# Optimization experiments

Hardware: AMD Instinct MI355X
Metric: run time of the kernel (lower is better)

Reference implementation:

```python
import jax, jax.numpy as jnp
import numpy as np

N = 100000
E = 1600000
D = 128          # in_feat == hidden_size
L = 3            # hidden layers
EPS = 1e-5       # BatchNorm1d eps


def setup_inputs() -> dict:
    key = jax.random.key(0)
    ks = jax.random.split(key, 12)
    x = jax.random.normal(ks[0], (N, D), dtype=jnp.float32)
    edge_index = jax.random.randint(ks[1], (2, E), 0, N, dtype=jnp.int64)
    s = 1.0 / np.sqrt(D)
    # stacked hidden-layer SAGEConv params: lin_l (neighbor), lin_r (root), bias on lin_l
    Wl = jax.random.uniform(ks[2], (L, D, D), jnp.float32, -s, s)
    Wr = jax.random.uniform(ks[3], (L, D, D), jnp.float32, -s, s)
    b = jax.random.uniform(ks[4], (L, D), jnp.float32, -s, s)
    # batchnorm affine params
    gamma = jnp.ones((L, D), jnp.float32)
    beta = jnp.zeros((L, D), jnp.float32)
    # output SAGEConv: D -> 1
    Wl_out = jax.random.uniform(ks[5], (D, 1), jnp.float32, -s, s)
    Wr_out = jax.random.uniform(ks[6], (D, 1), jnp.float32, -s, s)
    b_out = jax.random.uniform(ks[7], (1,), jnp.float32, -s, s)
    return {"x": x, "edge_index": edge_index, "Wl": Wl, "Wr": Wr, "b": b,
            "gamma": gamma, "beta": beta, "Wl_out": Wl_out, "Wr_out": Wr_out,
            "b_out": b_out}


def _sage(x, src, dst, inv_deg, Wl, Wr, b):
    # gather neighbor features along edges, mean-aggregate at destination
    msg_sum = jax.ops.segment_sum(x[src], dst, num_segments=N)   # [N, F]
    mean = msg_sum * inv_deg                                     # 0 for isolated nodes
    return mean @ Wl + x @ Wr + b


def _batchnorm(x, gamma, beta):
    m = jnp.mean(x, axis=0)
    v = jnp.mean((x - m) ** 2, axis=0)  # biased var, as torch BN uses for normalization
    return gamma * (x - m) * jax.lax.rsqrt(v + EPS) + beta


def reference(x, edge_index, Wl, Wr, b, gamma, beta, Wl_out, Wr_out, b_out):
    src, dst = edge_index[0], edge_index[1]
    deg = jax.ops.segment_sum(jnp.ones((E,), x.dtype), dst, num_segments=N)
    inv_deg = jnp.where(deg > 0, 1.0 / jnp.maximum(deg, 1.0), 0.0)[:, None]
    h = x
    for i in range(L):
        h = _sage(h, src, dst, inv_deg, Wl[i], Wr[i], b[i])
        h = jax.nn.relu(h)
        h = _batchnorm(h, gamma[i], beta[i])
    out = _sage(h, src, dst, inv_deg, Wl_out, Wr_out, b_out)
    return jax.nn.sigmoid(out)  # [N, 1]
```

## Files before the change

### kernel.cpp

```cpp
#include <hip/hip_runtime.h>

typedef unsigned short u16;
typedef unsigned int u32;
typedef unsigned long long u64;

#define GN 100000
#define GE 1600000
#define DCAP 64
#define NRANGE 196
#define NBKT (NRANGE * 8)
#define BCAP 1536
#define LDA 136

typedef __bf16 bf16x8 __attribute__((ext_vector_type(8)));
typedef float f32x4 __attribute__((ext_vector_type(4)));
typedef float f32x2 __attribute__((ext_vector_type(2)));
typedef u32 u32x4 __attribute__((ext_vector_type(4)));
typedef u32 u32x2 __attribute__((ext_vector_type(2)));

__device__ __forceinline__ float bl(u32 u){ return __uint_as_float(u << 16); }
__device__ __forceinline__ float bh(u32 u){ return __uint_as_float(u & 0xffff0000u); }
__device__ __forceinline__ float bfu(u16 v){ return __uint_as_float(((u32)v) << 16); }
__device__ __forceinline__ u16 f2bf(float f){
    u32 u = __float_as_uint(f);
    u32 r = (u + 0x7fffu + ((u >> 16) & 1u)) >> 16;
    return (u16)r;
}
__device__ __forceinline__ u32 pack2(float a, float b){
    return (u32)f2bf(a) | ((u32)f2bf(b) << 16);
}
__device__ __forceinline__ u32 pk8x4(float a, float b, float c, float d){
    u32 p = (u32)__builtin_amdgcn_cvt_pk_fp8_f32(a, b, 0, false);
    p = (u32)__builtin_amdgcn_cvt_pk_fp8_f32(c, d, p, true);
    return p;
}

__global__ void __launch_bounds__(256) k_init(const int* ei, const u32* xraw,
                                              int* cursor, float* colpart, int* flags,
                                              int* bcur){
    int i = blockIdx.x * 256 + threadIdx.x;
    if (i < GN) cursor[i] = 0;
    if (i < NBKT) bcur[i] = 0;
    if (i < 6144) colpart[i] = 0.f;
    int t = threadIdx.x;
    if (blockIdx.x == 0){
        __shared__ int s_any[4];
        int v = 0;
        #pragma unroll
        for (int j = 0; j < 4; ++j){
            int k = t * 4 + j;
            v |= ei[2 * k * 1000 + 1];
        }
        #pragma unroll
        for (int m = 1; m < 64; m <<= 1) v |= __shfl_xor(v, m);
        if ((t & 63) == 0) s_any[t >> 6] = v;
        __syncthreads();
        if (t == 0){
            int any = s_any[0] | s_any[1] | s_any[2] | s_any[3];
            flags[0] = (any == 0) ? 1 : 0;
        }
    }
    if (blockIdx.x == 1){
        __shared__ int s_cnt[4];
        int cnt = 0;
        #pragma unroll
        for (int j = 0; j < 4; ++j){
            int idx = (t * 4 + j) * 6000 + 3;
            u32 u = xraw[idx];
            int e = (u >> 7) & 0xFF;
            cnt += (e >= 100 && e <= 140) ? 1 : 0;
        }
        #pragma unroll
        for (int m = 1; m < 64; m <<= 1) cnt += __shfl_xor(cnt, m);
        if ((t & 63) == 0) s_cnt[t >> 6] = cnt;
        __syncthreads();
        if (t == 0){
            int tot = s_cnt[0] + s_cnt[1] + s_cnt[2] + s_cnt[3];
            flags[1] = (tot > 512) ? 0 : 1;
        }
    }
}

__global__ void __launch_bounds__(256) k_convx(const void* x, const int* flags,
                                               u16* xb, u32* h8){
    int tid = blockIdx.x * 256 + threadIdx.x;
    int node = tid >> 4, l15 = tid & 15;
    if (node >= GN) return;
    float f[8];
    if (flags[1]){
        const float* xf = (const float*)x + node * 128 + l15;
        #pragma unroll
        for (int a = 0; a < 8; ++a) f[a] = __builtin_nontemporal_load(xf + a * 16);
    } else {
        const u16* xh = (const u16*)x + node * 128 + l15;
        #pragma unroll
        for (int a = 0; a < 8; ++a) f[a] = bfu(xh[a * 16]);
    }
    u16* xo = xb + node * 128 + l15;
    #pragma unroll
    for (int a = 0; a < 8; ++a) xo[a * 16] = f2bf(f[a]);
    u32x2 e = { pk8x4(f[0], f[1], f[2], f[3]), pk8x4(f[4], f[5], f[6], f[7]) };
    ((u32x2*)h8)[node * 16 + l15] = e;
}

#define WOFF_WR    49152
#define WOFF_B     98304
#define WOFF_G     98688
#define WOFF_BE    99072
#define WOFF_WLO   99456
#define WOFF_WRO   99584
#define WOFF_BO    99712
#define WTOT       99713
__global__ void __launch_bounds__(256) k_convw(const void* Wl, const void* Wr, const void* b,
                                               const void* g, const void* be, const void* wlo,
                                               const void* wro, const void* bo,
                                               const int* flags, u16* wbuf, float* biasf){
    int i = blockIdx.x * 256 + threadIdx.x;
    if (i >= WTOT) return;
    const void* s; int k;
    if (i < WOFF_B){
        bool isWl = (i < WOFF_WR);
        const void* src = isWl ? Wl : Wr;
        int r = isWl ? i : i - WOFF_WR;
        int layer = r >> 14, L = r & 16383;
        int kk = isWl ? (((L & 7) << 4) | (L >> 10))
                      : (((L >> 10) << 3) | (L & 7));
        int cc = (L >> 3) & 127;
        int si = layer * 16384 + kk * 128 + cc;
        float fv = flags[1] ? ((const float*)src)[si] : bfu(((const u16*)src)[si]);
        wbuf[i] = f2bf(fv);
        return;
    }
    if      (i < WOFF_G  ){ s = b;   k = i - WOFF_B; }
    else if (i < WOFF_BE ){ s = g;   k = i - WOFF_G; }
    else if (i < WOFF_WLO){ s = be;  k = i - WOFF_BE; }
    else if (i < WOFF_WRO){ s = wlo; k = i - WOFF_WLO; }
    else if (i < WOFF_BO ){ s = wro; k = i - WOFF_WRO; }
    else                  { s = bo;  k = 0; }
    float fv = flags[1] ? ((const float*)s)[k] : bfu(((const u16*)s)[k]);
    wbuf[i] = f2bf(fv);
    if (i >= WOFF_B && i < WOFF_B + 384) biasf[i - WOFF_B] = fv;
}

__global__ void __launch_bounds__(256) k_fillA(const int* ei, const int* flags,
                                               int* bcur, u64* pairs){
    __shared__ int cnt[256];
    __shared__ int lofs[256];
    __shared__ int gbase[NRANGE];
    __shared__ int wsum[4];
    __shared__ u64 lp[1024];
    int t = threadIdx.x;
    int lane = t & 63, w = t >> 6;
    int res = blockIdx.x & 7;
    int base = blockIdx.x * 1024;
    int is64 = flags[0];
    cnt[t] = 0;
    __syncthreads();
    int myd[4], mys[4], slot[4], myr[4];
    #pragma unroll
    for (int j = 0; j < 4; ++j){
        int e = base + j * 256 + t;
        if (e < GE){
            int d, s;
            if (is64){ d = __builtin_nontemporal_load(ei + 2 * (GE + e));
                       s = __builtin_nontemporal_load(ei + 2 * e); }
            else     { d = __builtin_nontemporal_load(ei + GE + e);
                       s = __builtin_nontemporal_load(ei + e); }
            myd[j] = d; mys[j] = s; myr[j] = d >> 9;
            slot[j] = atomicAdd(&cnt[myr[j]], 1);
        } else myr[j] = -1;
    }
    __syncthreads();
    int v = cnt[t];
    int sv = v;
    #pragma unroll
    for (int d = 1; d < 64; d <<= 1){
        int u = __shfl_up(sv, d);
        if (lane >= d) sv += u;
    }
    if (lane == 63) wsum[w] = sv;
    __syncthreads();
    int prefix = 0;
    #pragma unroll
    for (int j = 0; j < 4; ++j) if (j < w) prefix += wsum[j];
    lofs[t] = sv + prefix - v;
    if (t < NRANGE && cnt[t] > 0)
        gbase[t] = atomicAdd(&bcur[t * 8 + res], cnt[t]);
    __syncthreads();
    #pragma unroll
    for (int j = 0; j < 4; ++j){
        if (myr[j] >= 0)
            lp[lofs[myr[j]] + slot[j]] = ((u64)(u32)myd[j] << 32) | (u32)mys[j];
    }
    __syncthreads();
    int total = GE - base; if (total > 1024) total = 1024;
    for (int i = t; i < total; i += 256){
        u64 pr = lp[i];
        int r = (int)(pr >> 32) >> 9;
        int g = gbase[r] + (i - lofs[r]);
        if (g < BCAP) pairs[((size_t)(r * 8 + res)) * BCAP + g] = pr;
    }
}

__global__ void __launch_bounds__(256) k_fillB(const int* bcur, const u64* pairs,
                                               int* cursor, int* col){
    int range = blockIdx.x % 200;
    int sub   = blockIdx.x / 200;
    if (range >= NRANGE || sub >= 8) return;
    int bkt = range * 8 + sub;
    int n = bcur[bkt]; if (n > BCAP) n = BCAP;
    const u64* P = pairs + (size_t)bkt * BCAP;
    for (int i = threadIdx.x; i < n; i += 256){
        u64 pr = __builtin_nontemporal_load(P + i);
        int s = (int)(u32)pr, d = (int)(pr >> 32);
        int pos = atomicAdd(&cursor[d], 1);
        if (pos < DCAP) col[d * DCAP + pos] = s;
    }
}

__global__ void __launch_bounds__(256, 4) k_gemm(const u32* h8, const int* deg, const int* col,
                                                 const u16* hin,
                                                 const u16* Wlp, const u16* Wrp,
                                                 const float* biasf, u16* hout,
                                                 u32* h8o, int write8, float* colpart){
    __shared__ u16 smA[128 * LDA];
    __shared__ float sst[256];
    int t = threadIdx.x;
    int wid = t >> 6, lane = t & 63;
    int quad = lane >> 4, l15 = lane & 15;
    int r0 = blockIdx.x * 128;
    sst[t] = 0.f;

    {
        int g = t >> 4, lg = t & 15;
        const u32x2* hrow = (const u32x2*)h8;
        #define ACC8(v) { \
            A01 += __builtin_amdgcn_cvt_pk_f32_fp8((v).x, false); \
            A23 += __builtin_amdgcn_cvt_pk_f32_fp8((v).x, true);  \
            A45 += __builtin_amdgcn_cvt_pk_f32_fp8((v).y, false); \
            A67 += __builtin_amdgcn_cvt_pk_f32_fp8((v).y, true); }
        for (int m = 0; m < 8; ++m){
            int lr = g + (m << 4);
            int node = r0 + lr;
            f32x2 A01 = {0.f,0.f}, A23 = {0.f,0.f}, A45 = {0.f,0.f}, A67 = {0.f,0.f};
            int d = 0;
            if (node < GN){
                d = deg[node];
                int cnt = d < DCAP ? d : DCAP;
                const int* nb = col + node * DCAP;
                int e = 0;
                for (; e + 7 < cnt; e += 8){
                    u32x2 v0 = hrow[(size_t)nb[e]     * 16 + lg];
                    u32x2 v1 = hrow[(size_t)nb[e + 1] * 16 + lg];
                    u32x2 v2 = hrow[(size_t)nb[e + 2] * 16 + lg];
                    u32x2 v3 = hrow[(size_t)nb[e + 3] * 16 + lg];
                    u32x2 v4 = hrow[(size_t)nb[e + 4] * 16 + lg];
                    u32x2 v5 = hrow[(size_t)nb[e + 5] * 16 + lg];
                    u32x2 v6 = hrow[(size_t)nb[e + 6] * 16 + lg];
                    u32x2 v7 = hrow[(size_t)nb[e + 7] * 16 + lg];
                    ACC8(v0) ACC8(v1) ACC8(v2) ACC8(v3) ACC8(v4) ACC8(v5) ACC8(v6) ACC8(v7)
                }
                for (; e + 1 < cnt; e += 2){
                    u32x2 v0 = hrow[(size_t)nb[e]     * 16 + lg];
                    u32x2 v1 = hrow[(size_t)nb[e + 1] * 16 + lg];
                    ACC8(v0) ACC8(v1)
                }
                if (e < cnt){
                    u32x2 v0 = hrow[(size_t)nb[e] * 16 + lg];
                    ACC8(v0)
                }
            }
            float inv = (d > 0) ? 1.f / (float)d : 0.f;
            f32x2 iv = {inv, inv};
            A01 *= iv; A23 *= iv; A45 *= iv; A67 *= iv;
            u32x4 o;
            o.x = pack2(A01.x, A01.y); o.y = pack2(A23.x, A23.y);
            o.z = pack2(A45.x, A45.y); o.w = pack2(A67.x, A67.y);
            *(u32x4*)(smA + lr * LDA + lg * 8) = o;
        }
        #undef ACC8
    }
    __syncthreads();

    f32x4 acc[2][8];
    #pragma unroll
    for (int i = 0; i < 2; i++)
        #pragma unroll
        for (int j = 0; j < 8; j++) acc[i][j] = (f32x4){0.f, 0.f, 0.f, 0.f};

    int node0 = r0 + wid * 32 + l15, node1 = node0 + 16;

    {
        const u32x4* Wg = (const u32x4*)Wlp;
        const u16* a0 = smA + (wid * 32 + l15) * LDA;
        const u16* a1 = a0 + 16 * LDA;
        #pragma unroll
        for (int s = 0; s < 4; ++s){
            int kc = (s << 2) + quad;
            union { u32x4 u; bf16x8 v; } fa0, fa1;
            fa0.u = *(const u32x4*)(a0 + (kc << 3));
            fa1.u = *(const u32x4*)(a1 + (kc << 3));
            const u32x4* wg = Wg + (kc << 7) + l15;
            #pragma unroll
            for (int cb = 0; cb < 8; ++cb){
                union { u32x4 u; bf16x8 v; } fw;
                fw.u = wg[cb << 4];
                acc[0][cb] = __builtin_amdgcn_mfma_f32_16x16x32_bf16(fa0.v, fw.v, acc[0][cb], 0, 0, 0);
                acc[1][cb] = __builtin_amdgcn_mfma_f32_16x16x32_bf16(fa1.v, fw.v, acc[1][cb], 0, 0, 0);
            }
        }
    }
    {
        const u32x4* Wg = (const u32x4*)Wrp;
        #pragma unroll
        for (int s = 0; s < 4; ++s){
            int kk = (s << 5) + (quad << 3);
            union { u32x4 u; bf16x8 v; } fa0, fa1;
            fa0.u = (node0 < GN) ? *(const u32x4*)(hin + node0 * 128 + kk) : (u32x4){0,0,0,0};
            fa1.u = (node1 < GN) ? *(const u32x4*)(hin + node1 * 128 + kk) : (u32x4){0,0,0,0};
            int kc = (s << 2) + quad;
            const u32x4* wg = Wg + (kc << 7) + l15;
            #pragma unroll
            for (int cb = 0; cb < 8; ++cb){
                union { u32x4 u; bf16x8 v; } fw;
                fw.u = wg[cb << 4];
                acc[0][cb] = __builtin_amdgcn_mfma_f32_16x16x32_bf16(fa0.v, fw.v, acc[0][cb], 0, 0, 0);
                acc[1][cb] = __builtin_amdgcn_mfma_f32_16x16x32_bf16(fa1.v, fw.v, acc[1][cb], 0, 0, 0);
            }
        }
    }

    float bsv[8];
    #pragma unroll
    for (int cb = 0; cb < 8; cb++) bsv[cb] = biasf[cb * 16 + l15];
    float csum[8], csq[8];
    #pragma unroll
    for (int cb = 0; cb < 8; cb++){ csum[cb] = 0.f; csq[cb] = 0.f; }

    #pragma unroll
    for (int rb = 0; rb < 2; ++rb){
        #pragma unroll
        for (int rr = 0; rr < 4; ++rr){
            int row = r0 + wid * 32 + rb * 16 + quad * 4 + rr;
            float v[8];
            #pragma unroll
            for (int cb = 0; cb < 8; ++cb) v[cb] = fmaxf(acc[rb][cb][rr] + bsv[cb], 0.f);
            if (row < GN){
                #pragma unroll
                for (int cb = 0; cb < 8; ++cb){
                    hout[row * 128 + cb * 16 + l15] = f2bf(v[cb]);
                    csum[cb] += v[cb]; csq[cb] += v[cb] * v[cb];
                }
                if (write8){
                    u32x2 pp = { pk8x4(v[0], v[1], v[2], v[3]),
                                 pk8x4(v[4], v[5], v[6], v[7]) };
                    ((u32x2*)h8o)[row * 16 + l15] = pp;
                }
            }
        }
    }
    #pragma unroll
    for (int cb = 0; cb < 8; cb++){
        float cs = csum[cb], cq = csq[cb];
        cs += __shfl_xor(cs, 16); cs += __shfl_xor(cs, 32);
        cq += __shfl_xor(cq, 16); cq += __shfl_xor(cq, 32);
        if (quad == 0){
            atomicAdd(&sst[cb * 16 + l15], cs);
            atomicAdd(&sst[128 + cb * 16 + l15], cq);
        }
    }
    __syncthreads();
    atomicAdd(&colpart[(blockIdx.x & 7) * 256 + t], sst[t]);
}

__global__ void __launch_bounds__(256) k_bnf(const float* colpart, const u16* gamma, const u16* beta,
                                             int mode,
                                             const u16* WlN, const u16* WrN, u16* wfd,
                                             const float* bNsrc, float* bNdst,
                                             const u16* wlo, const u16* wro, const u16* bo,
                                             u16* hwl, u16* hwr, float* hb){
    __shared__ float s_sc[128], s_sh[128], s_red[256];
    int t = threadIdx.x, b = blockIdx.x;
    if (t < 128){
        float s = 0.f, q = 0.f;
        #pragma unroll
        for (int j = 0; j < 8; ++j){
            s += colpart[j * 256 + t];
            q += colpart[j * 256 + 128 + t];
        }
        const float invn = 1.f / (float)GN;
        float mean = s * invn;
        float var = fmaxf(q * invn - mean * mean, 0.f);
        float rstd = rsqrtf(var + 1e-5f);
        float g  = bfu(gamma[t]);
        float be = bfu(beta[t]);
        float sc = g * rstd, sh = be - mean * sc;
        s_sc[t] = sc; s_sh[t] = sh;
    }
    __syncthreads();
    if (mode == 0){
        if (b < 64){
            int idx = b * 256 + t;
            int kl = ((idx & 7) << 4) | (idx >> 10);
            int kr = ((idx >> 10) << 3) | (idx & 7);
            wfd[idx]         = f2bf(s_sc[kl] * bfu(WlN[idx]));
            wfd[16384 + idx] = f2bf(s_sc[kr] * bfu(WrN[idx]));
        } else if (t < 128){
            float acc = bNsrc[t];
            for (int k = 0; k < 128; ++k){
                int Ll = ((k & 15) << 10) + (t << 3) + (k >> 4);
                int Lr = ((k >> 3) << 10) + (t << 3) + (k & 7);
                acc += s_sh[k] * (bfu(WlN[Ll]) + bfu(WrN[Lr]));
            }
            bNdst[t] = acc;
        }
    } else if (b == 64){
        float contrib = 0.f;
        if (t < 128){
            float wl = bfu(wlo[t]), wr = bfu(wro[t]);
            hwl[t] = f2bf(s_sc[t] * wl);
            hwr[t] = f2bf(s_sc[t] * wr);
            contrib = s_sh[t] * (wl + wr);
        }
        s_red[t] = contrib;
        __syncthreads();
        for (int off = 128; off >= 1; off >>= 1){
            if (t < off) s_red[t] += s_red[t + off];
            __syncthreads();
        }
        if (t == 0) hb[0] = s_red[0] + bfu(bo[0]);
    }
}

__global__ void __launch_bounds__(256) k_dot(const u16* h, const u16* wl, const u16* wr,
                                             float* y, float* r){
    int node = (blockIdx.x * 256 + threadIdx.x) >> 6;
    int lane = threadIdx.x & 63;
    if (node >= GN) return;
    u32 hv  = ((const u32*)h)[node * 64 + lane];
    u32 wlv = ((const u32*)wl)[lane];
    u32 wrv = ((const u32*)wr)[lane];
    float hlo = bl(hv), hhi = bh(hv);
    float ya = hlo * bl(wlv) + hhi * bh(wlv);
    float ra = hlo * bl(wrv) + hhi * bh(wrv);
    #pragma unroll
    for (int m = 1; m < 64; m <<= 1){ ya += __shfl_xor(ya, m); ra += __shfl_xor(ra, m); }
    if (lane == 0){ y[node] = ya; r[node] = ra; }
}

__global__ void __launch_bounds__(256) k_out(const float* y, const float* r, const int* deg,
                                             const int* col, const float* hb,
                                             const int* flags, void* out){
    int n = blockIdx.x * 256 + threadIdx.x;
    if (n >= GN) return;
    int d = deg[n];
    int cnt = d < DCAP ? d : DCAP;
    const int* nb = col + n * DCAP;
    float s = 0.f;
    for (int e = 0; e < cnt; ++e) s += y[nb[e]];
    float inv = (d > 0) ? 1.f / (float)d : 0.f;
    float z = inv * s + r[n] + hb[0];
    float sg = 1.f / (1.f + __expf(-z));
    if (flags[1]) ((float*)out)[n] = sg;
    else          ((u16*)out)[n] = f2bf(sg);
}

extern "C" void kernel_launch(void* const* d_in, const int* in_sizes, int n_in,
                              void* d_out, int out_size, void* d_ws, size_t ws_size,
                              hipStream_t stream) {
    const void* x     = d_in[0];
    const int*  ei    = (const int*)d_in[1];
    const void* Wl    = d_in[2];
    const void* Wr    = d_in[3];
    const void* bias  = d_in[4];
    const void* gamma = d_in[5];
    const void* beta  = d_in[6];
    const void* wlout = d_in[7];
    const void* wrout = d_in[8];
    const void* bout  = d_in[9];

    char* p = (char*)d_ws;
    auto take = [&](size_t b){ void* q = (void*)p; p += (b + 255) & ~(size_t)255; return q; };
    int*   cursor = (int*)  take((size_t)GN * 4);
    int*   flags  = (int*)  take(256);
    int*   bcur   = (int*)  take((size_t)NBKT * 4);
    float* colpart= (float*)take(6144 * 4);
    float* biasf  = (float*)take(384 * 4);
    float* bf2    = (float*)take(128 * 4);
    float* bf3    = (float*)take(128 * 4);
    float* hb     = (float*)take(256);
    u16*   wf2    = (u16*)  take(32768 * 2);
    u16*   wf3    = (u16*)  take(32768 * 2);
    u16*   hwl    = (u16*)  take(128 * 2);
    u16*   hwr    = (u16*)  take(128 * 2);
    float* yv     = (float*)take((size_t)GN * 4);
    float* rv     = (float*)take((size_t)GN * 4);
    int*   col    = (int*)  take((size_t)GN * DCAP * 4);
    u16*   xb     = (u16*)  take((size_t)GN * 128 * 2);
    u16*   hbuf   = (u16*)  take((size_t)GN * 128 * 2);
    u32*   h8a    = (u32*)  take((size_t)GN * 128);
    u32*   h8b    = (u32*)  take((size_t)GN * 128);
    u64*   pairs  = (u64*)  take((size_t)NBKT * BCAP * 8);
    u16*   wbuf   = (u16*)  take((size_t)WTOT * 2);

    const int NB_N = (GN + 255) / 256;
    const int NB_W = (GN + 3) / 4;
    const int NB_G = (GN + 127) / 128;
    const int NB_M = (GN * 16 + 255) / 256;
    const int NB_C = (WTOT + 255) / 256;
    const int NB_A = (GE + 1023) / 1024;

    k_init <<<NB_N, 256, 0, stream>>>(ei, (const u32*)x, cursor, colpart, flags, bcur);
    k_convx<<<NB_M, 256, 0, stream>>>(x, flags, xb, h8a);
    k_convw<<<NB_C, 256, 0, stream>>>(Wl, Wr, bias, gamma, beta, wlout, wrout, bout, flags, wbuf, biasf);
    k_fillA<<<NB_A, 256, 0, stream>>>(ei, flags, bcur, pairs);
    k_fillB<<<1600, 256, 0, stream>>>(bcur, pairs, cursor, col);

    const u16* hin = xb;
    for (int i = 0; i < 3; ++i){
        const u16* Wlp; const u16* Wrp; const float* bfi;
        if (i == 0){ Wlp = wbuf;     Wrp = wbuf + WOFF_WR; bfi = biasf; }
        else if (i == 1){ Wlp = wf2; Wrp = wf2 + 16384;    bfi = bf2; }
        else { Wlp = wf3;            Wrp = wf3 + 16384;    bfi = bf3; }
        u16* wfd = (i == 0) ? wf2 : wf3;
        float* bNdst = (i == 0) ? bf2 : bf3;
        int nx = (i < 2) ? (i + 1) : 0;
        const u32* h8i = (i == 1) ? h8b : h8a;
        u32*       h8o = (i == 0) ? h8b : h8a;
        k_gemm<<<NB_G, 256, 0, stream>>>(h8i, cursor, col, hin, Wlp, Wrp, bfi,
                                         hbuf, (i == 2) ? h8b : h8o, (i < 2) ? 1 : 0,
                                         colpart + i * 2048);
        k_bnf <<<65, 256, 0, stream>>>(colpart + i * 2048,
            wbuf + WOFF_G + i * 128, wbuf + WOFF_BE + i * 128, (i == 2) ? 1 : 0,
            wbuf + nx * 16384, wbuf + WOFF_WR + nx * 16384, wfd,
            biasf + nx * 128, bNdst,
            wbuf + WOFF_WLO, wbuf + WOFF_WRO, wbuf + WOFF_BO, hwl, hwr, hb);
        hin = hbuf;
    }
    k_dot<<<NB_W, 256, 0, stream>>>(hbuf, hwl, hwr, yv, rv);
    k_out<<<NB_N, 256, 0, stream>>>(yv, rv, cursor, col, hb, flags, d_out);
}
```

Measured before the change: 459.0 us.

## Shrink GEMM tile to 64 rows with per-wave gather and no block barriers

Rows per block in the fused aggregate+GEMM kernel drop from 128 to 64. Each wave now gathers its own 16 rows with 16-byte fp8 loads (8 lanes per row), so the LDS tile is wave-private and the __syncthreads becomes a waitcnt. Column statistics are atomically added straight to global partials instead of going through a shared-memory reduction. This lowers LDS use and synchronisation to raise occupancy and latency hiding for the gather. In exchange, each B-fragment load now feeds half as many MFMAs, and there are more global atomics.

```diff
diff --git a/kernel.cpp b/kernel.cpp
--- a/kernel.cpp
+++ b/kernel.cpp
@@ -223,26 +223,31 @@
                                                  const u16* Wlp, const u16* Wrp,
                                                  const float* biasf, u16* hout,
                                                  u32* h8o, int write8, float* colpart){
-    __shared__ u16 smA[128 * LDA];
-    __shared__ float sst[256];
+    __shared__ u16 smA[64 * LDA];
     int t = threadIdx.x;
     int wid = t >> 6, lane = t & 63;
     int quad = lane >> 4, l15 = lane & 15;
-    int r0 = blockIdx.x * 128;
-    sst[t] = 0.f;
+    int r0 = blockIdx.x * 64;
+    int wr0 = wid * 16;
 
     {
-        int g = t >> 4, lg = t & 15;
-        const u32x2* hrow = (const u32x2*)h8;
-        #define ACC8(v) { \
-            A01 += __builtin_amdgcn_cvt_pk_f32_fp8((v).x, false); \
-            A23 += __builtin_amdgcn_cvt_pk_f32_fp8((v).x, true);  \
-            A45 += __builtin_amdgcn_cvt_pk_f32_fp8((v).y, false); \
-            A67 += __builtin_amdgcn_cvt_pk_f32_fp8((v).y, true); }
-        for (int m = 0; m < 8; ++m){
-            int lr = g + (m << 4);
+        int g8 = lane >> 3, lg8 = lane & 7;
+        const u32x4* hrow4 = (const u32x4*)h8;
+        #define ACC16(v) { \
+            a01 += __builtin_amdgcn_cvt_pk_f32_fp8((v).x, false); \
+            a23 += __builtin_amdgcn_cvt_pk_f32_fp8((v).x, true);  \
+            a45 += __builtin_amdgcn_cvt_pk_f32_fp8((v).y, false); \
+            a67 += __builtin_amdgcn_cvt_pk_f32_fp8((v).y, true);  \
+            b01 += __builtin_amdgcn_cvt_pk_f32_fp8((v).z, false); \
+            b23 += __builtin_amdgcn_cvt_pk_f32_fp8((v).z, true);  \
+            b45 += __builtin_amdgcn_cvt_pk_f32_fp8((v).w, false); \
+            b67 += __builtin_amdgcn_cvt_pk_f32_fp8((v).w, true); }
+        #pragma unroll
+        for (int m = 0; m < 2; ++m){
+            int lr = wr0 + (g8 << 1) + m;
             int node = r0 + lr;
-            f32x2 A01 = {0.f,0.f}, A23 = {0.f,0.f}, A45 = {0.f,0.f}, A67 = {0.f,0.f};
+            f32x2 a01 = {0.f,0.f}, a23 = {0.f,0.f}, a45 = {0.f,0.f}, a67 = {0.f,0.f};
+            f32x2 b01 = {0.f,0.f}, b23 = {0.f,0.f}, b45 = {0.f,0.f}, b67 = {0.f,0.f};
             int d = 0;
             if (node < GN){
                 d = deg[node];
@@ -250,63 +255,65 @@
                 const int* nb = col + node * DCAP;
                 int e = 0;
                 for (; e + 7 < cnt; e += 8){
-                    u32x2 v0 = hrow[(size_t)nb[e]     * 16 + lg];
-                    u32x2 v1 = hrow[(size_t)nb[e + 1] * 16 + lg];
-                    u32x2 v2 = hrow[(size_t)nb[e + 2] * 16 + lg];
-                    u32x2 v3 = hrow[(size_t)nb[e + 3] * 16 + lg];
-                    u32x2 v4 = hrow[(size_t)nb[e + 4] * 16 + lg];
-                    u32x2 v5 = hrow[(size_t)nb[e + 5] * 16 + lg];
-                    u32x2 v6 = hrow[(size_t)nb[e + 6] * 16 + lg];
-                    u32x2 v7 = hrow[(size_t)nb[e + 7] * 16 + lg];
-                    ACC8(v0) ACC8(v1) ACC8(v2) ACC8(v3) ACC8(v4) ACC8(v5) ACC8(v6) ACC8(v7)
+                    u32x4 v0 = hrow4[(size_t)nb[e]     * 8 + lg8];
+                    u32x4 v1 = hrow4[(size_t)nb[e + 1] * 8 + lg8];
+                    u32x4 v2 = hrow4[(size_t)nb[e + 2] * 8 + lg8];
+                    u32x4 v3 = hrow4[(size_t)nb[e + 3] * 8 + lg8];
+                    u32x4 v4 = hrow4[(size_t)nb[e + 4] * 8 + lg8];
+                    u32x4 v5 = hrow4[(size_t)nb[e + 5] * 8 + lg8];
+                    u32x4 v6 = hrow4[(size_t)nb[e + 6] * 8 + lg8];
+                    u32x4 v7 = hrow4[(size_t)nb[e + 7] * 8 + lg8];
+                    ACC16(v0) ACC16(v1) ACC16(v2) ACC16(v3)
+                    ACC16(v4) ACC16(v5) ACC16(v6) ACC16(v7)
                 }
                 for (; e + 1 < cnt; e += 2){
-                    u32x2 v0 = hrow[(size_t)nb[e]     * 16 + lg];
-                    u32x2 v1 = hrow[(size_t)nb[e + 1] * 16 + lg];
-                    ACC8(v0) ACC8(v1)
+                    u32x4 v0 = hrow4[(size_t)nb[e]     * 8 + lg8];
+                    u32x4 v1 = hrow4[(size_t)nb[e + 1] * 8 + lg8];
+                    ACC16(v0) ACC16(v1)
                 }
                 if (e < cnt){
-                    u32x2 v0 = hrow[(size_t)nb[e] * 16 + lg];
-                    ACC8(v0)
+                    u32x4 v0 = hrow4[(size_t)nb[e] * 8 + lg8];
+                    ACC16(v0)
                 }
             }
             float inv = (d > 0) ? 1.f / (float)d : 0.f;
             f32x2 iv = {inv, inv};
-            A01 *= iv; A23 *= iv; A45 *= iv; A67 *= iv;
-            u32x4 o;
-            o.x = pack2(A01.x, A01.y); o.y = pack2(A23.x, A23.y);
-            o.z = pack2(A45.x, A45.y); o.w = pack2(A67.x, A67.y);
-            *(u32x4*)(smA + lr * LDA + lg * 8) = o;
-        }
-        #undef ACC8
-    }
-    __syncthreads();
-
-    f32x4 acc[2][8];
-    #pragma unroll
-    for (int i = 0; i < 2; i++)
-        #pragma unroll
-        for (int j = 0; j < 8; j++) acc[i][j] = (f32x4){0.f, 0.f, 0.f, 0.f};
-
-    int node0 = r0 + wid * 32 + l15, node1 = node0 + 16;
+            a01 *= iv; a23 *= iv; a45 *= iv; a67 *= iv;
+            b01 *= iv; b23 *= iv; b45 *= iv; b67 *= iv;
+            u32x4 o0, o1;
+            o0.x = pack2(a01.x, a01.y); o0.y = pack2(a23.x, a23.y);
+            o0.z = pack2(a45.x, a45.y); o0.w = pack2(a67.x, a67.y);
+            o1.x = pack2(b01.x, b01.y); o1.y = pack2(b23.x, b23.y);
+            o1.z = pack2(b45.x, b45.y); o1.w = pack2(b67.x, b67.y);
+            u16* wp = smA + lr * LDA + (lg8 << 4);
+            *(u32x4*)wp = o0;
+            *(u32x4*)(wp + 8) = o1;
+        }
+        #undef ACC16
+    }
+    __asm__ volatile("s_waitcnt lgkmcnt(0)" ::: "memory");
+    __builtin_amdgcn_sched_barrier(0);
+
+    f32x4 acc[8];
+    #pragma unroll
+    for (int j = 0; j < 8; j++) acc[j] = (f32x4){0.f, 0.f, 0.f, 0.f};
+
+    int node0 = r0 + wr0 + l15;
 
     {
         const u32x4* Wg = (const u32x4*)Wlp;
-        const u16* a0 = smA + (wid * 32 + l15) * LDA;
-        const u16* a1 = a0 + 16 * LDA;
+        const u16* a0 = smA + (wr0 + l15) * LDA;
         #pragma unroll
         for (int s = 0; s < 4; ++s){
             int kc = (s << 2) + quad;
-            union { u32x4 u; bf16x8 v; } fa0, fa1;
+            union { u32x4 u; bf16x8 v; } fa0;
             fa0.u = *(const u32x4*)(a0 + (kc << 3));
-            fa1.u = *(const u32x4*)(a1 + (kc << 3));
             const u32x4* wg = Wg + (kc << 7) + l15;
             #pragma unroll
             for (int cb = 0; cb < 8; ++cb){
                 union { u32x4 u; bf16x8 v; } fw;
                 fw.u = wg[cb << 4];
-                acc[0][cb] = __builtin_amdgcn_mfma_f32_16x16x32_bf16(fa0.v, fw.v, acc[0][cb], 0, 0, 0);
-                acc[1][cb] = __builtin_amdgcn_mfma_f32_16x16x32_bf16(fa1.v, fw.v, acc[1][cb], 0, 0, 0);
+                acc[cb] = __builtin_amdgcn_mfma_f32_16x16x32_bf16(fa0.v, fw.v, acc[cb], 0, 0, 0);
             }
         }
     }
@@ -315,17 +322,15 @@
         #pragma unroll
         for (int s = 0; s < 4; ++s){
             int kk = (s << 5) + (quad << 3);
-            union { u32x4 u; bf16x8 v; } fa0, fa1;
+            union { u32x4 u; bf16x8 v; } fa0;
             fa0.u = (node0 < GN) ? *(const u32x4*)(hin + node0 * 128 + kk) : (u32x4){0,0,0,0};
-            fa1.u = (node1 < GN) ? *(const u32x4*)(hin + node1 * 128 + kk) : (u32x4){0,0,0,0};
             int kc = (s << 2) + quad;
             const u32x4* wg = Wg + (kc << 7) + l15;
             #pragma unroll
             for (int cb = 0; cb < 8; ++cb){
                 union { u32x4 u; bf16x8 v; } fw;
                 fw.u = wg[cb << 4];
-                acc[0][cb] = __builtin_amdgcn_mfma_f32_16x16x32_bf16(fa0.v, fw.v, acc[0][cb], 0, 0, 0);
-                acc[1][cb] = __builtin_amdgcn_mfma_f32_16x16x32_bf16(fa1.v, fw.v, acc[1][cb], 0, 0, 0);
+                acc[cb] = __builtin_amdgcn_mfma_f32_16x16x32_bf16(fa0.v, fw.v, acc[cb], 0, 0, 0);
             }
         }
     }
@@ -338,39 +343,35 @@
     for (int cb = 0; cb < 8; cb++){ csum[cb] = 0.f; csq[cb] = 0.f; }
 
     #pragma unroll
-    for (int rb = 0; rb < 2; ++rb){
-        #pragma unroll
-        for (int rr = 0; rr < 4; ++rr){
-            int row = r0 + wid * 32 + rb * 16 + quad * 4 + rr;
-            float v[8];
+    for (int rr = 0; rr < 4; ++rr){
+        int row = r0 + wr0 + quad * 4 + rr;
+        float v[8];
+        #pragma unroll
+        for (int cb = 0; cb < 8; ++cb) v[cb] = fmaxf(acc[cb][rr] + bsv[cb], 0.f);
+        if (row < GN){
             #pragma unroll
-            for (int cb = 0; cb < 8; ++cb) v[cb] = fmaxf(acc[rb][cb][rr] + bsv[cb], 0.f);
-            if (row < GN){
-                #pragma unroll
-                for (int cb = 0; cb < 8; ++cb){
-                    hout[row * 128 + cb * 16 + l15] = f2bf(v[cb]);
-                    csum[cb] += v[cb]; csq[cb] += v[cb] * v[cb];
-                }
-                if (write8){
-                    u32x2 pp = { pk8x4(v[0], v[1], v[2], v[3]),
-                                 pk8x4(v[4], v[5], v[6], v[7]) };
-                    ((u32x2*)h8o)[row * 16 + l15] = pp;
-                }
+            for (int cb = 0; cb < 8; ++cb){
+                hout[row * 128 + cb * 16 + l15] = f2bf(v[cb]);
+                csum[cb] += v[cb]; csq[cb] += v[cb] * v[cb];
             }
-        }
-    }
+            if (write8){
+                u32x2 pp = { pk8x4(v[0], v[1], v[2], v[3]),
+                             pk8x4(v[4], v[5], v[6], v[7]) };
+                ((u32x2*)h8o)[row * 16 + l15] = pp;
+            }
+        }
+    }
+    int base = (blockIdx.x & 7) * 256;
     #pragma unroll
     for (int cb = 0; cb < 8; cb++){
         float cs = csum[cb], cq = csq[cb];
         cs += __shfl_xor(cs, 16); cs += __shfl_xor(cs, 32);
         cq += __shfl_xor(cq, 16); cq += __shfl_xor(cq, 32);
         if (quad == 0){
-            atomicAdd(&sst[cb * 16 + l15], cs);
-            atomicAdd(&sst[128 + cb * 16 + l15], cq);
-        }
-    }
-    __syncthreads();
-    atomicAdd(&colpart[(blockIdx.x & 7) * 256 + t], sst[t]);
+            atomicAdd(&colpart[base + cb * 16 + l15], cs);
+            atomicAdd(&colpart[base + 128 + cb * 16 + l15], cq);
+        }
+    }
 }
 
 __global__ void __launch_bounds__(256) k_bnf(const float* colpart, const u16* gamma, const u16* beta,
@@ -505,7 +506,7 @@
 
     const int NB_N = (GN + 255) / 256;
     const int NB_W = (GN + 3) / 4;
-    const int NB_G = (GN + 127) / 128;
+    const int NB_G = (GN + 63) / 64;
     const int NB_M = (GN * 16 + 255) / 256;
     const int NB_C = (WTOT + 255) / 256;
     const int NB_A = (GE + 1023) / 1024;
```

After: 458.4 us. No clear change (-0.1%).
